# Performance work log

Hardware: AMD Instinct MI355X
Metric: run time of the kernel (lower is better)

The kernel has to match this reference:

```python
import jax, jax.numpy as jnp
import numpy as np

B, S, T = 32, 512, 512
SRC_SIZE, TGT_SIZE, OUT_SIZE, NUM_HEAD = 2048, 1024, 1024, 8
HEAD_DIM = OUT_SIZE // NUM_HEAD  # 128


def setup_inputs() -> dict:
    key = jax.random.key(0)
    ks = jax.random.split(key, 12)
    src = jax.random.normal(ks[0], (B, S, SRC_SIZE), dtype=jnp.float32)
    tgt = jax.random.normal(ks[1], (B, T, TGT_SIZE), dtype=jnp.float32)
    # binary float masks (1=valid, 0=pad); guarantee at least one valid src per row
    src_mask = (jax.random.uniform(ks[2], (B, S)) > 0.3).astype(jnp.float32)
    src_mask = src_mask.at[:, 0].set(1.0)
    tgt_mask = (jax.random.uniform(ks[3], (B, T)) > 0.3).astype(jnp.float32)
    tgt_mask = tgt_mask.at[:, 0].set(1.0)
    # FCNet in this repo is weight_norm(Linear) with no activation at drop=0 -> plain Linear
    def lin(k, out_f, in_f):
        return jax.random.normal(k, (out_f, in_f), dtype=jnp.float32) / np.sqrt(in_f)
    W_src = lin(ks[4], 2 * OUT_SIZE, SRC_SIZE)
    b_src = jnp.zeros((2 * OUT_SIZE,), jnp.float32)
    W_tgt = lin(ks[5], OUT_SIZE, TGT_SIZE)
    b_tgt = jnp.zeros((OUT_SIZE,), jnp.float32)
    W_out = lin(ks[6], OUT_SIZE, OUT_SIZE + TGT_SIZE)
    b_out = jnp.zeros((OUT_SIZE,), jnp.float32)
    return {"src": src, "tgt": tgt, "src_mask": src_mask, "tgt_mask": tgt_mask,
            "W_src": W_src, "b_src": b_src, "W_tgt": W_tgt, "b_tgt": b_tgt,
            "W_out": W_out, "b_out": b_out}


def reference(src, tgt, src_mask, tgt_mask, W_src, b_src, W_tgt, b_tgt, W_out, b_out):
    b, s, _ = src.shape
    t = tgt.shape[1]
    # projections (FCNet == Linear here)
    src_trans = jnp.einsum('bsf,of->bso', src, W_src) + b_src        # [B,S,2D]
    tgt_trans = jnp.einsum('btf,of->bto', tgt, W_tgt) + b_tgt        # [B,T,D]
    src_trans = src_trans * src_mask[:, :, None]
    tgt_trans = tgt_trans * tgt_mask[:, :, None]
    src_key, src_val = jnp.split(src_trans, 2, axis=2)               # each [B,S,D]
    # contiguous per-head chunks == reshape
    k = src_key.reshape(b, s, NUM_HEAD, HEAD_DIM)
    v = src_val.reshape(b, s, NUM_HEAD, HEAD_DIM)
    q = tgt_trans.reshape(b, t, NUM_HEAD, HEAD_DIM)
    scores = jnp.einsum('bthd,bshd->bhts', q, k) / np.sqrt(HEAD_DIM)  # [B,H,T,S]
    scores = jnp.where(src_mask[:, None, None, :] == 0, -jnp.inf, scores)
    attn = jax.nn.softmax(scores, axis=-1)
    tgt_update = jnp.einsum('bhts,bshd->bthd', attn, v).reshape(b, t, OUT_SIZE)
    cat_tgt = jnp.concatenate([tgt, tgt_update], axis=2)             # [B,T,TGT+D]
    return jnp.einsum('btf,of->bto', cat_tgt, W_out) + b_out         # [B,T,D]
```

## Files before the change

kernel.cpp:

```cpp
#include <hip/hip_runtime.h>

typedef __attribute__((ext_vector_type(4))) float f32x4;
typedef __attribute__((ext_vector_type(8))) short short8;
typedef unsigned short u16;

#define SB0() __builtin_amdgcn_sched_barrier(0)

__device__ __forceinline__ u16 f2bf(float f) {
  unsigned int u = __float_as_uint(f);
  return (u16)((u + 0x7fffu + ((u >> 16) & 1u)) >> 16);
}

__device__ __forceinline__ void gload16(const void* g, void* l) {
  __builtin_amdgcn_global_load_lds((const __attribute__((address_space(1))) void*)g,
                                   (__attribute__((address_space(3))) void*)l, 16, 0, 0);
}

__global__ void cvt_f32_bf16(const float* __restrict__ in, u16* __restrict__ out, int n4) {
  int i = blockIdx.x * blockDim.x + threadIdx.x;
  int stride = gridDim.x * blockDim.x;
  for (; i < n4; i += stride) {
    float4 v = ((const float4*)in)[i];
    ushort4 o;
    o.x = f2bf(v.x); o.y = f2bf(v.y); o.z = f2bf(v.z); o.w = f2bf(v.w);
    ((ushort4*)out)[i] = o;
  }
}

__global__ void cvt_tgt_strided(const float* __restrict__ in, u16* __restrict__ cat, int n4) {
  int i = blockIdx.x * blockDim.x + threadIdx.x;
  int stride = gridDim.x * blockDim.x;
  for (; i < n4; i += stride) {
    int e = i * 4;
    int row = e >> 10;
    int c = e & 1023;
    float4 v = ((const float4*)in)[i];
    ushort4 o;
    o.x = f2bf(v.x); o.y = f2bf(v.y); o.z = f2bf(v.z); o.w = f2bf(v.w);
    *(ushort4*)(cat + (size_t)row * 2048 + c) = o;
  }
}

template <bool MASK, bool OUTBF, bool VSPLIT>
__global__ __launch_bounds__(512) void gemm256(const u16* __restrict__ A, int lda,
                                               const u16* __restrict__ W,
                                               const float* __restrict__ bias,
                                               const float* __restrict__ rowmask,
                                               void* __restrict__ Cout, int ldc,
                                               int nbn, int K,
                                               u16* __restrict__ vTout) {
  __shared__ __align__(16) u16 lds[2 * 32768];
  const int tid = threadIdx.x;
  const int lane = tid & 63;
  const int wid = tid >> 6;
  const int lr = lane & 15, lh = lane >> 4;
  const int wm = wid >> 2;
  const int wn = wid & 3;

  const int nwg = gridDim.x;
  const int cpx = nwg >> 3;
  const int bid = (blockIdx.x & 7) * cpx + (blockIdx.x >> 3);
  const int bm = bid / nbn;
  const int bn = bid - bm * nbn;

  const int srow = tid >> 3;
  const int scol = ((tid & 7) ^ (srow & 7)) << 3;
  const u16* As0 = A + (size_t)(bm * 256 + srow) * lda + scol;
  const u16* Ws0 = W + (size_t)(bn * 256 + srow) * K + scol;

  auto stageA = [&](int h, int t, int buf) {
    char* d = (char*)lds + buf * 65536 + h * 16384 + tid * 16;
    const u16* s = As0 + (size_t)(h * 128) * lda + t * 64;
    gload16(s, d);
    gload16(s + (size_t)64 * lda, d + 8192);
  };
  auto stageB = [&](int h, int t, int buf) {
    char* d = (char*)lds + buf * 65536 + 32768 + h * 16384 + tid * 16;
    const u16* s = Ws0 + (size_t)(h * 128) * K + t * 64;
    gload16(s, d);
    gload16(s + (size_t)64 * K, d + 8192);
  };

  const int key = (lr & 7) << 4;
  const int sb0 = ((0 + lh) << 4) ^ key;
  const int sb1 = ((4 + lh) << 4) ^ key;
  const int arow = (wm * 64 + lr) * 128;
  const int brow = 32768 + (wn * 32 + lr) * 128;

  f32x4 acc[8][4];
#pragma unroll
  for (int m = 0; m < 8; ++m)
#pragma unroll
    for (int n = 0; n < 4; ++n) acc[m][n] = (f32x4){0.f, 0.f, 0.f, 0.f};

  const int NT = K >> 6;

  stageA(0, 0, 0); stageB(0, 0, 0); stageB(1, 0, 0); stageA(1, 0, 0);
  asm volatile("s_waitcnt vmcnt(0)" ::: "memory");
  __builtin_amdgcn_s_barrier();
  SB0();

  for (int t = 0; t < NT; ++t) {
    const int cur = t & 1, nxt = cur ^ 1;
    const char* Lb = (const char*)lds + cur * 65536;
    const bool pf = (t + 1 < NT);

    short8 a[4][2], a2[4][2], b0[2][2], b1[2][2];

#pragma unroll
    for (int m = 0; m < 4; ++m) {
      a[m][0] = *(const short8*)(Lb + arow + m * 2048 + sb0);
      a[m][1] = *(const short8*)(Lb + arow + m * 2048 + sb1);
    }
#pragma unroll
    for (int n = 0; n < 2; ++n) {
      b0[n][0] = *(const short8*)(Lb + brow + n * 2048 + sb0);
      b0[n][1] = *(const short8*)(Lb + brow + n * 2048 + sb1);
    }
    SB0();
    if (pf) { stageA(0, t + 1, nxt); stageB(0, t + 1, nxt);
              stageB(1, t + 1, nxt); stageA(1, t + 1, nxt); }
#pragma unroll
    for (int n = 0; n < 2; ++n) {
      b1[n][0] = *(const short8*)(Lb + brow + 16384 + n * 2048 + sb0);
      b1[n][1] = *(const short8*)(Lb + brow + 16384 + n * 2048 + sb1);
    }
    SB0();
    asm volatile("s_waitcnt lgkmcnt(4)" ::: "memory");
    SB0();
    __builtin_amdgcn_s_setprio(1);
#pragma unroll
    for (int m = 0; m < 4; ++m)
#pragma unroll
      for (int n = 0; n < 2; ++n) {
        acc[m][n] = __builtin_amdgcn_mfma_f32_16x16x32_bf16(a[m][0], b0[n][0], acc[m][n], 0, 0, 0);
        acc[m][n] = __builtin_amdgcn_mfma_f32_16x16x32_bf16(a[m][1], b0[n][1], acc[m][n], 0, 0, 0);
      }
    __builtin_amdgcn_s_setprio(0);
#pragma unroll
    for (int m = 0; m < 4; ++m) {
      a2[m][0] = *(const short8*)(Lb + 16384 + arow + m * 2048 + sb0);
      a2[m][1] = *(const short8*)(Lb + 16384 + arow + m * 2048 + sb1);
    }
    asm volatile("s_waitcnt lgkmcnt(8)" ::: "memory");
    SB0();
    __builtin_amdgcn_s_setprio(1);
#pragma unroll
    for (int m = 0; m < 4; ++m)
#pragma unroll
      for (int n = 0; n < 2; ++n) {
        acc[m][2 + n] = __builtin_amdgcn_mfma_f32_16x16x32_bf16(a[m][0], b1[n][0], acc[m][2 + n], 0, 0, 0);
        acc[m][2 + n] = __builtin_amdgcn_mfma_f32_16x16x32_bf16(a[m][1], b1[n][1], acc[m][2 + n], 0, 0, 0);
      }
    __builtin_amdgcn_s_setprio(0);
    asm volatile("s_waitcnt lgkmcnt(0)" ::: "memory");
    SB0();
    __builtin_amdgcn_s_setprio(1);
#pragma unroll
    for (int m = 0; m < 4; ++m)
#pragma unroll
      for (int n = 0; n < 2; ++n) {
        acc[4 + m][n] = __builtin_amdgcn_mfma_f32_16x16x32_bf16(a2[m][0], b0[n][0], acc[4 + m][n], 0, 0, 0);
        acc[4 + m][n] = __builtin_amdgcn_mfma_f32_16x16x32_bf16(a2[m][1], b0[n][1], acc[4 + m][n], 0, 0, 0);
      }
#pragma unroll
    for (int m = 0; m < 4; ++m)
#pragma unroll
      for (int n = 0; n < 2; ++n) {
        acc[4 + m][2 + n] = __builtin_amdgcn_mfma_f32_16x16x32_bf16(a2[m][0], b1[n][0], acc[4 + m][2 + n], 0, 0, 0);
        acc[4 + m][2 + n] = __builtin_amdgcn_mfma_f32_16x16x32_bf16(a2[m][1], b1[n][1], acc[4 + m][2 + n], 0, 0, 0);
      }
    __builtin_amdgcn_s_setprio(0);
    SB0();
    asm volatile("s_waitcnt vmcnt(0)" ::: "memory");
    __builtin_amdgcn_s_barrier();
    SB0();
  }

  const int r0 = bm * 256 + wm * 64 + lh * 4;
  const int c0 = bn * 256 + wn * 32 + lr;

  if constexpr (VSPLIT) {
    if (bn * 256 >= 1024) {
#pragma unroll
      for (int mi = 0; mi < 8; ++mi) {
        const int row_base = r0 + (mi >> 2) * 128 + (mi & 3) * 16;
        const int b = row_base >> 9;
        const int s = row_base & 511;
        float mk[4];
#pragma unroll
        for (int i = 0; i < 4; ++i) mk[i] = rowmask[row_base + i];
#pragma unroll
        for (int ni = 0; ni < 4; ++ni) {
          const int col = c0 + (ni >> 1) * 128 + (ni & 1) * 16;
          const float bv = bias[col];
          const int vcol = col - 1024;
          u16* vp = vTout + ((size_t)(b * 8 + (vcol >> 7)) * 128 + (vcol & 127)) * 512 + s;
          ushort4 o;
          o.x = f2bf((acc[mi][ni][0] + bv) * mk[0]);
          o.y = f2bf((acc[mi][ni][1] + bv) * mk[1]);
          o.z = f2bf((acc[mi][ni][2] + bv) * mk[2]);
          o.w = f2bf((acc[mi][ni][3] + bv) * mk[3]);
          *(ushort4*)vp = o;
        }
      }
      return;
    }
  }

#pragma unroll
  for (int mi = 0; mi < 8; ++mi) {
    const int row_base = r0 + (mi >> 2) * 128 + (mi & 3) * 16;
#pragma unroll
    for (int i = 0; i < 4; ++i) {
      const int row = row_base + i;
      float msk = 1.f;
      if constexpr (MASK) msk = rowmask[row];
#pragma unroll
      for (int ni = 0; ni < 4; ++ni) {
        const int col = c0 + (ni >> 1) * 128 + (ni & 1) * 16;
        float v = (acc[mi][ni][i] + bias[col]) * msk;
        if constexpr (OUTBF)
          ((u16*)Cout)[(size_t)row * ldc + col] = f2bf(v);
        else
          ((float*)Cout)[(size_t)row * ldc + col] = v;
      }
    }
  }
}

__global__ __launch_bounds__(256) void attn_fwd(const u16* __restrict__ q,
                                                const u16* __restrict__ kbuf,
                                                const u16* __restrict__ vT,
                                                const float* __restrict__ smask,
                                                u16* __restrict__ cat) {
  __shared__ __align__(16) u16 lds[20480];
  u16* Ks = lds;
  u16* Vt = lds + 8192;
  u16* Ps = lds + 16384;
  const int tid = threadIdx.x;
  const int lane = tid & 63;
  const int w = tid >> 6;
  const int lr = lane & 15, lh = lane >> 4;
  const int bh = blockIdx.x & 255;
  const int qb = blockIdx.x >> 8;
  const int b = bh >> 3;
  const int h = bh & 7;
  const int t0 = qb * 64 + w * 16;
  const float SCALE = 0.08838834764831845f;

  const u16* kbase = kbuf + (size_t)(b * 512) * 1024 + h * 128;
  const u16* vbase = vT + (size_t)bh * 128 * 512;

  short8 qf[4];
  {
    const u16* qp = q + (size_t)(b * 512 + t0 + lr) * 1024 + h * 128 + lh * 8;
#pragma unroll
    for (int kc = 0; kc < 4; ++kc) qf[kc] = *(const short8*)(qp + kc * 32);
  }

  f32x4 o[8];
#pragma unroll
  for (int dt = 0; dt < 8; ++dt) o[dt] = (f32x4){0.f, 0.f, 0.f, 0.f};
  float m_run[4], l_run[4];
#pragma unroll
  for (int i = 0; i < 4; ++i) { m_run[i] = -1e30f; l_run[i] = 0.f; }

  for (int s0 = 0; s0 < 512; s0 += 64) {
    __syncthreads();
#pragma unroll
    for (int it = 0; it < 4; ++it) {
      int idx = it * 256 + tid;
      int kr = idx >> 4, ks = idx & 15;
      gload16(kbase + (size_t)(s0 + kr) * 1024 + ((ks ^ (kr & 7)) * 8), (char*)Ks + idx * 16);
      int vr = idx >> 3, vs = idx & 7;
      gload16(vbase + (size_t)vr * 512 + s0 + ((vs ^ (vr & 7)) * 8), (char*)Vt + idx * 16);
    }
    asm volatile("s_waitcnt vmcnt(0)" ::: "memory");
    __syncthreads();

    f32x4 sc[4];
#pragma unroll
    for (int st = 0; st < 4; ++st) {
      f32x4 c = (f32x4){0.f, 0.f, 0.f, 0.f};
      const int row = st * 16 + lr;
#pragma unroll
      for (int kc = 0; kc < 4; ++kc) {
        short8 kb = *(const short8*)((const char*)Ks + row * 256 +
                                     ((kc * 64 + lh * 16) ^ ((row & 7) << 4)));
        c = __builtin_amdgcn_mfma_f32_16x16x32_bf16(qf[kc], kb, c, 0, 0, 0);
      }
      sc[st] = c;
    }

    float cm[4];
#pragma unroll
    for (int st = 0; st < 4; ++st) cm[st] = smask[b * 512 + s0 + st * 16 + lr];

    float pv[4][4], mx[4];
#pragma unroll
    for (int i = 0; i < 4; ++i) mx[i] = -1e30f;
#pragma unroll
    for (int st = 0; st < 4; ++st)
#pragma unroll
      for (int i = 0; i < 4; ++i) {
        float v = (cm[st] != 0.f) ? sc[st][i] * SCALE : -1e30f;
        pv[st][i] = v;
        mx[i] = fmaxf(mx[i], v);
      }
#pragma unroll
    for (int off = 1; off < 16; off <<= 1)
#pragma unroll
      for (int i = 0; i < 4; ++i) mx[i] = fmaxf(mx[i], __shfl_xor(mx[i], off));

    float m_new[4], scl[4], rs[4];
#pragma unroll
    for (int i = 0; i < 4; ++i) {
      m_new[i] = fmaxf(m_run[i], mx[i]);
      scl[i] = __expf(m_run[i] - m_new[i]);
      rs[i] = 0.f;
    }
#pragma unroll
    for (int st = 0; st < 4; ++st)
#pragma unroll
      for (int i = 0; i < 4; ++i) {
        float p = (cm[st] != 0.f) ? __expf(pv[st][i] - m_new[i]) : 0.f;
        pv[st][i] = p;
        rs[i] += p;
      }
#pragma unroll
    for (int off = 1; off < 16; off <<= 1)
#pragma unroll
      for (int i = 0; i < 4; ++i) rs[i] += __shfl_xor(rs[i], off);
#pragma unroll
    for (int i = 0; i < 4; ++i) {
      l_run[i] = l_run[i] * scl[i] + rs[i];
      m_run[i] = m_new[i];
    }
#pragma unroll
    for (int dt = 0; dt < 8; ++dt)
#pragma unroll
      for (int i = 0; i < 4; ++i) o[dt][i] *= scl[i];

#pragma unroll
    for (int st = 0; st < 4; ++st)
#pragma unroll
      for (int i = 0; i < 4; ++i) {
        const int prow = lh * 4 + i;
        Ps[w * 1024 + prow * 64 + (((st * 2 + (lr >> 3)) ^ (prow & 7)) * 8) + (lr & 7)] =
            f2bf(pv[st][i]);
      }

    short8 pa[2];
#pragma unroll
    for (int s2 = 0; s2 < 2; ++s2)
      pa[s2] = *(const short8*)(Ps + w * 1024 + lr * 64 + (((s2 * 4 + lh) ^ (lr & 7)) * 8));
#pragma unroll
    for (int dt = 0; dt < 8; ++dt) {
#pragma unroll
      for (int s2 = 0; s2 < 2; ++s2) {
        const int row = dt * 16 + lr;
        short8 vb = *(const short8*)((const char*)Vt + row * 128 +
                                     ((s2 * 64 + lh * 16) ^ ((row & 7) << 4)));
        o[dt] = __builtin_amdgcn_mfma_f32_16x16x32_bf16(pa[s2], vb, o[dt], 0, 0, 0);
      }
    }
  }

  float inv[4];
#pragma unroll
  for (int i = 0; i < 4; ++i) inv[i] = 1.f / l_run[i];
  u16* outp = cat + (size_t)(b * 512 + t0 + lh * 4) * 2048 + 1024 + h * 128 + lr;
#pragma unroll
  for (int dt = 0; dt < 8; ++dt)
#pragma unroll
    for (int i = 0; i < 4; ++i)
      outp[(size_t)i * 2048 + dt * 16] = f2bf(o[dt][i] * inv[i]);
}

extern "C" void kernel_launch(void* const* d_in, const int* in_sizes, int n_in,
                              void* d_out, int out_size, void* d_ws, size_t ws_size,
                              hipStream_t stream) {
  (void)in_sizes; (void)n_in; (void)out_size; (void)ws_size;
  const float* src      = (const float*)d_in[0];
  const float* tgt      = (const float*)d_in[1];
  const float* src_mask = (const float*)d_in[2];
  const float* tgt_mask = (const float*)d_in[3];
  const float* W_src    = (const float*)d_in[4];
  const float* b_src    = (const float*)d_in[5];
  const float* W_tgt    = (const float*)d_in[6];
  const float* b_tgt    = (const float*)d_in[7];
  const float* W_out    = (const float*)d_in[8];
  const float* b_out    = (const float*)d_in[9];

  char* ws = (char*)d_ws;
  u16* catb = (u16*)(ws);
  u16* kbuf = (u16*)(ws + 67108864);
  u16* vTb  = (u16*)(ws + 100663296);
  u16* qbuf = (u16*)(ws + 134217728);
  u16* wsrc = (u16*)(ws + 167772160);
  u16* wtgt = (u16*)(ws + 176160768);
  u16* wout = (u16*)(ws + 178257920);

  cvt_f32_bf16<<<2048, 256, 0, stream>>>(src, catb, 16384 * 2048 / 4);
  cvt_f32_bf16<<<1024, 256, 0, stream>>>(W_src, wsrc, 2048 * 2048 / 4);
  cvt_f32_bf16<<<256, 256, 0, stream>>>(W_tgt, wtgt, 1024 * 1024 / 4);
  cvt_f32_bf16<<<512, 256, 0, stream>>>(W_out, wout, 1024 * 2048 / 4);

  gemm256<true, true, true><<<512, 512, 0, stream>>>(catb, 2048, wsrc, b_src, src_mask,
                                                     kbuf, 1024, 8, 2048, vTb);

  cvt_tgt_strided<<<1024, 256, 0, stream>>>(tgt, catb, 16384 * 1024 / 4);

  gemm256<true, true, false><<<256, 512, 0, stream>>>(catb, 2048, wtgt, b_tgt, tgt_mask,
                                                      qbuf, 1024, 4, 1024, nullptr);

  attn_fwd<<<2048, 256, 0, stream>>>(qbuf, kbuf, vTb, src_mask, catb);

  gemm256<false, false, false><<<256, 512, 0, stream>>>(catb, 2048, wout, b_out, nullptr,
                                                        (float*)d_out, 1024, 4, 2048, nullptr);
}
```

Baseline: 384.2 us.

## Prefetch next-tile LDS fragments inside GEMM loop and enlarge attention blocks

The GEMM main loop is restructured so that the A and B0 register fragments for the next K tile are read from LDS during the current iteration, after an early barrier, instead of at the top of the next iteration. This is meant to hide LDS read latency behind the MFMAs. Separately, the attention kernel moves to 512-thread blocks covering 128 query rows, so each K/V tile staged in LDS is shared by twice as many queries and half as many blocks are launched. The attention change needs more LDS per block, which may lower occupancy, and the extra barrier placement in the GEMM adds synchronisation risk.

```diff
diff --git a/kernel.cpp b/kernel.cpp
--- a/kernel.cpp
+++ b/kernel.cpp
@@ -100,13 +100,9 @@
   __builtin_amdgcn_s_barrier();
   SB0();
 
-  for (int t = 0; t < NT; ++t) {
-    const int cur = t & 1, nxt = cur ^ 1;
-    const char* Lb = (const char*)lds + cur * 65536;
-    const bool pf = (t + 1 < NT);
-
-    short8 a[4][2], a2[4][2], b0[2][2], b1[2][2];
-
+  short8 a[4][2], a2[4][2], b0[2][2], b1[2][2];
+  {
+    const char* Lb = (const char*)lds;
 #pragma unroll
     for (int m = 0; m < 4; ++m) {
       a[m][0] = *(const short8*)(Lb + arow + m * 2048 + sb0);
@@ -118,8 +114,17 @@
       b0[n][1] = *(const short8*)(Lb + brow + n * 2048 + sb1);
     }
     SB0();
-    if (pf) { stageA(0, t + 1, nxt); stageB(0, t + 1, nxt);
+  }
+
+  for (int t = 0; t < NT; ++t) {
+    const int nxt = (t + 1) & 1;
+    const char* Lb = (const char*)lds + (t & 1) * 65536;
+    const char* Ln = (const char*)lds + nxt * 65536;
+    const bool ra = (t + 1 < NT);
+
+    if (ra) { stageA(0, t + 1, nxt); stageB(0, t + 1, nxt);
               stageB(1, t + 1, nxt); stageA(1, t + 1, nxt); }
+
 #pragma unroll
     for (int n = 0; n < 2; ++n) {
       b1[n][0] = *(const short8*)(Lb + brow + 16384 + n * 2048 + sb0);
@@ -137,11 +142,14 @@
         acc[m][n] = __builtin_amdgcn_mfma_f32_16x16x32_bf16(a[m][1], b0[n][1], acc[m][n], 0, 0, 0);
       }
     __builtin_amdgcn_s_setprio(0);
+    SB0();
+
 #pragma unroll
     for (int m = 0; m < 4; ++m) {
       a2[m][0] = *(const short8*)(Lb + 16384 + arow + m * 2048 + sb0);
       a2[m][1] = *(const short8*)(Lb + 16384 + arow + m * 2048 + sb1);
     }
+    SB0();
     asm volatile("s_waitcnt lgkmcnt(8)" ::: "memory");
     SB0();
     __builtin_amdgcn_s_setprio(1);
@@ -153,8 +161,24 @@
         acc[m][2 + n] = __builtin_amdgcn_mfma_f32_16x16x32_bf16(a[m][1], b1[n][1], acc[m][2 + n], 0, 0, 0);
       }
     __builtin_amdgcn_s_setprio(0);
-    asm volatile("s_waitcnt lgkmcnt(0)" ::: "memory");
-    SB0();
+    SB0();
+
+    if (ra) {
+      asm volatile("s_waitcnt vmcnt(0)" ::: "memory");
+      __builtin_amdgcn_s_barrier();
+      SB0();
+#pragma unroll
+      for (int m = 0; m < 4; ++m) {
+        a[m][0] = *(const short8*)(Ln + arow + m * 2048 + sb0);
+        a[m][1] = *(const short8*)(Ln + arow + m * 2048 + sb1);
+      }
+      SB0();
+      asm volatile("s_waitcnt lgkmcnt(8)" ::: "memory");
+      SB0();
+    } else {
+      asm volatile("s_waitcnt lgkmcnt(0)" ::: "memory");
+      SB0();
+    }
     __builtin_amdgcn_s_setprio(1);
 #pragma unroll
     for (int m = 0; m < 4; ++m)
@@ -163,6 +187,18 @@
         acc[4 + m][n] = __builtin_amdgcn_mfma_f32_16x16x32_bf16(a2[m][0], b0[n][0], acc[4 + m][n], 0, 0, 0);
         acc[4 + m][n] = __builtin_amdgcn_mfma_f32_16x16x32_bf16(a2[m][1], b0[n][1], acc[4 + m][n], 0, 0, 0);
       }
+    __builtin_amdgcn_s_setprio(0);
+    SB0();
+
+    if (ra) {
+#pragma unroll
+      for (int n = 0; n < 2; ++n) {
+        b0[n][0] = *(const short8*)(Ln + brow + n * 2048 + sb0);
+        b0[n][1] = *(const short8*)(Ln + brow + n * 2048 + sb1);
+      }
+      SB0();
+    }
+    __builtin_amdgcn_s_setprio(1);
 #pragma unroll
     for (int m = 0; m < 4; ++m)
 #pragma unroll
@@ -172,7 +208,6 @@
       }
     __builtin_amdgcn_s_setprio(0);
     SB0();
-    asm volatile("s_waitcnt vmcnt(0)" ::: "memory");
     __builtin_amdgcn_s_barrier();
     SB0();
   }
@@ -229,12 +264,12 @@
   }
 }
 
-__global__ __launch_bounds__(256) void attn_fwd(const u16* __restrict__ q,
+__global__ __launch_bounds__(512) void attn_fwd(const u16* __restrict__ q,
                                                 const u16* __restrict__ kbuf,
                                                 const u16* __restrict__ vT,
                                                 const float* __restrict__ smask,
                                                 u16* __restrict__ cat) {
-  __shared__ __align__(16) u16 lds[20480];
+  __shared__ __align__(16) u16 lds[24576];
   u16* Ks = lds;
   u16* Vt = lds + 8192;
   u16* Ps = lds + 16384;
@@ -246,7 +281,7 @@
   const int qb = blockIdx.x >> 8;
   const int b = bh >> 3;
   const int h = bh & 7;
-  const int t0 = qb * 64 + w * 16;
+  const int t0 = qb * 128 + w * 16;
   const float SCALE = 0.08838834764831845f;
 
   const u16* kbase = kbuf + (size_t)(b * 512) * 1024 + h * 128;
@@ -269,8 +304,8 @@
   for (int s0 = 0; s0 < 512; s0 += 64) {
     __syncthreads();
 #pragma unroll
-    for (int it = 0; it < 4; ++it) {
-      int idx = it * 256 + tid;
+    for (int it = 0; it < 2; ++it) {
+      int idx = it * 512 + tid;
       int kr = idx >> 4, ks = idx & 15;
       gload16(kbase + (size_t)(s0 + kr) * 1024 + ((ks ^ (kr & 7)) * 8), (char*)Ks + idx * 16);
       int vr = idx >> 3, vs = idx & 7;
@@ -415,7 +450,7 @@
   gemm256<true, true, false><<<256, 512, 0, stream>>>(catb, 2048, wtgt, b_tgt, tgt_mask,
                                                       qbuf, 1024, 4, 1024, nullptr);
 
-  attn_fwd<<<2048, 256, 0, stream>>>(qbuf, kbuf, vTb, src_mask, catb);
+  attn_fwd<<<1024, 512, 0, stream>>>(qbuf, kbuf, vTb, src_mask, catb);
 
   gemm256<false, false, false><<<256, 512, 0, stream>>>(catb, 2048, wout, b_out, nullptr,
                                                         (float*)d_out, 1024, 4, 2048, nullptr);
```

New measurement: 411.1 us. 1.07x slower.

## Pre-pack weights into MFMA fragment order and load B directly to registers

Applied to the files above, without the earlier changes.

Adds a pack_w kernel that converts the weight matrices to bf16 in the lane-ordered layout of the MFMA B operand. The GEMM then loads B fragments straight from global memory into registers, prefetched one step ahead, instead of staging them through LDS. This halves LDS use per block and removes the B LDS reads and writes. It also drops the XCD-aware block swizzle in favour of a simple bn/bm split. The risks are longer global-load latency on B, higher register pressure, and possibly worse L2 locality without the swizzle.

```diff
diff --git a/kernel.cpp b/kernel.cpp
--- a/kernel.cpp
+++ b/kernel.cpp
@@ -41,15 +41,34 @@
   }
 }
 
+__global__ void pack_w(const float* __restrict__ W, u16* __restrict__ Wp, int K, int total) {
+  int ci = blockIdx.x * 256 + threadIdx.x;
+  if (ci >= total) return;
+  int l = ci & 63;
+  int g = ci >> 6;
+  int K5 = K >> 5;
+  int np = g / K5;
+  int ksg = g - np * K5;
+  const float* s = W + (size_t)(np * 16 + (l & 15)) * K + ksg * 32 + (l >> 4) * 8;
+  float4 v0 = *(const float4*)s;
+  float4 v1 = *(const float4*)(s + 4);
+  u16* d = Wp + (size_t)ci * 8;
+  ushort4 o0, o1;
+  o0.x = f2bf(v0.x); o0.y = f2bf(v0.y); o0.z = f2bf(v0.z); o0.w = f2bf(v0.w);
+  o1.x = f2bf(v1.x); o1.y = f2bf(v1.y); o1.z = f2bf(v1.z); o1.w = f2bf(v1.w);
+  *(ushort4*)d = o0;
+  *(ushort4*)(d + 4) = o1;
+}
+
 template <bool MASK, bool OUTBF, bool VSPLIT>
 __global__ __launch_bounds__(512) void gemm256(const u16* __restrict__ A, int lda,
-                                               const u16* __restrict__ W,
+                                               const u16* __restrict__ Wp,
                                                const float* __restrict__ bias,
                                                const float* __restrict__ rowmask,
                                                void* __restrict__ Cout, int ldc,
-                                               int nbn, int K,
+                                               int nbnl, int K,
                                                u16* __restrict__ vTout) {
-  __shared__ __align__(16) u16 lds[2 * 32768];
+  __shared__ __align__(16) u16 lds[2 * 16384];
   const int tid = threadIdx.x;
   const int lane = tid & 63;
   const int wid = tid >> 6;
@@ -57,35 +76,34 @@
   const int wm = wid >> 2;
   const int wn = wid & 3;
 
-  const int nwg = gridDim.x;
-  const int cpx = nwg >> 3;
-  const int bid = (blockIdx.x & 7) * cpx + (blockIdx.x >> 3);
-  const int bm = bid / nbn;
-  const int bn = bid - bm * nbn;
+  const int bn = blockIdx.x & ((1 << nbnl) - 1);
+  const int bm = blockIdx.x >> nbnl;
 
   const int srow = tid >> 3;
   const int scol = ((tid & 7) ^ (srow & 7)) << 3;
   const u16* As0 = A + (size_t)(bm * 256 + srow) * lda + scol;
-  const u16* Ws0 = W + (size_t)(bn * 256 + srow) * K + scol;
-
-  auto stageA = [&](int h, int t, int buf) {
-    char* d = (char*)lds + buf * 65536 + h * 16384 + tid * 16;
-    const u16* s = As0 + (size_t)(h * 128) * lda + t * 64;
-    gload16(s, d);
-    gload16(s + (size_t)64 * lda, d + 8192);
+
+  auto stageA = [&](int t, int buf) {
+    char* d = (char*)lds + buf * 32768 + tid * 16;
+    const u16* s = As0 + t * 64;
+#pragma unroll
+    for (int i = 0; i < 4; ++i)
+      gload16(s + (size_t)(i * 64) * lda, d + i * 8192);
   };
-  auto stageB = [&](int h, int t, int buf) {
-    char* d = (char*)lds + buf * 65536 + 32768 + h * 16384 + tid * 16;
-    const u16* s = Ws0 + (size_t)(h * 128) * K + t * 64;
-    gload16(s, d);
-    gload16(s + (size_t)64 * K, d + 8192);
-  };
 
   const int key = (lr & 7) << 4;
-  const int sb0 = ((0 + lh) << 4) ^ key;
+  const int sb0 = (lh << 4) ^ key;
   const int sb1 = ((4 + lh) << 4) ^ key;
   const int arow = (wm * 64 + lr) * 128;
-  const int brow = 32768 + (wn * 32 + lr) * 128;
+
+  const int K5 = K >> 5;
+  const short8* Wp8 = (const short8*)Wp;
+  const short8* WB[2][2];
+#pragma unroll
+  for (int nh = 0; nh < 2; ++nh)
+#pragma unroll
+    for (int n = 0; n < 2; ++n)
+      WB[nh][n] = Wp8 + (size_t)(bn * 16 + nh * 8 + wn * 2 + n) * K5 * 64 + lane;
 
   f32x4 acc[8][4];
 #pragma unroll
@@ -95,55 +113,58 @@
 
   const int NT = K >> 6;
 
-  stageA(0, 0, 0); stageB(0, 0, 0); stageB(1, 0, 0); stageA(1, 0, 0);
+  short8 a[4][2], a2[4][2], b0[2][2], b1[2][2];
+
+  stageA(0, 0);
+  SB0();
+#pragma unroll
+  for (int n = 0; n < 2; ++n) {
+    b0[n][0] = WB[0][n][0];
+    b0[n][1] = WB[0][n][64];
+  }
+  SB0();
+#pragma unroll
+  for (int n = 0; n < 2; ++n) {
+    b1[n][0] = WB[1][n][0];
+    b1[n][1] = WB[1][n][64];
+  }
+  SB0();
   asm volatile("s_waitcnt vmcnt(0)" ::: "memory");
   __builtin_amdgcn_s_barrier();
   SB0();
 
   for (int t = 0; t < NT; ++t) {
-    const int cur = t & 1, nxt = cur ^ 1;
-    const char* Lb = (const char*)lds + cur * 65536;
+    const char* Lb = (const char*)lds + (t & 1) * 32768;
     const bool pf = (t + 1 < NT);
-
-    short8 a[4][2], a2[4][2], b0[2][2], b1[2][2];
 
 #pragma unroll
     for (int m = 0; m < 4; ++m) {
       a[m][0] = *(const short8*)(Lb + arow + m * 2048 + sb0);
       a[m][1] = *(const short8*)(Lb + arow + m * 2048 + sb1);
     }
-#pragma unroll
-    for (int n = 0; n < 2; ++n) {
-      b0[n][0] = *(const short8*)(Lb + brow + n * 2048 + sb0);
-      b0[n][1] = *(const short8*)(Lb + brow + n * 2048 + sb1);
-    }
-    SB0();
-    if (pf) { stageA(0, t + 1, nxt); stageB(0, t + 1, nxt);
-              stageB(1, t + 1, nxt); stageA(1, t + 1, nxt); }
-#pragma unroll
-    for (int n = 0; n < 2; ++n) {
-      b1[n][0] = *(const short8*)(Lb + brow + 16384 + n * 2048 + sb0);
-      b1[n][1] = *(const short8*)(Lb + brow + 16384 + n * 2048 + sb1);
-    }
-    SB0();
-    asm volatile("s_waitcnt lgkmcnt(4)" ::: "memory");
-    SB0();
-    __builtin_amdgcn_s_setprio(1);
-#pragma unroll
-    for (int m = 0; m < 4; ++m)
-#pragma unroll
-      for (int n = 0; n < 2; ++n) {
-        acc[m][n] = __builtin_amdgcn_mfma_f32_16x16x32_bf16(a[m][0], b0[n][0], acc[m][n], 0, 0, 0);
-        acc[m][n] = __builtin_amdgcn_mfma_f32_16x16x32_bf16(a[m][1], b0[n][1], acc[m][n], 0, 0, 0);
-      }
-    __builtin_amdgcn_s_setprio(0);
+    SB0();
 #pragma unroll
     for (int m = 0; m < 4; ++m) {
       a2[m][0] = *(const short8*)(Lb + 16384 + arow + m * 2048 + sb0);
       a2[m][1] = *(const short8*)(Lb + 16384 + arow + m * 2048 + sb1);
     }
+    SB0();
+    if (pf) stageA(t + 1, (t + 1) & 1);
+    SB0();
+
     asm volatile("s_waitcnt lgkmcnt(8)" ::: "memory");
     SB0();
+    __builtin_amdgcn_s_setprio(1);
+#pragma unroll
+    for (int m = 0; m < 4; ++m)
+#pragma unroll
+      for (int n = 0; n < 2; ++n) {
+        acc[m][n] = __builtin_amdgcn_mfma_f32_16x16x32_bf16(a[m][0], b0[n][0], acc[m][n], 0, 0, 0);
+        acc[m][n] = __builtin_amdgcn_mfma_f32_16x16x32_bf16(a[m][1], b0[n][1], acc[m][n], 0, 0, 0);
+      }
+    __builtin_amdgcn_s_setprio(0);
+    SB0();
+
     __builtin_amdgcn_s_setprio(1);
 #pragma unroll
     for (int m = 0; m < 4; ++m)
@@ -153,6 +174,8 @@
         acc[m][2 + n] = __builtin_amdgcn_mfma_f32_16x16x32_bf16(a[m][1], b1[n][1], acc[m][2 + n], 0, 0, 0);
       }
     __builtin_amdgcn_s_setprio(0);
+    SB0();
+
     asm volatile("s_waitcnt lgkmcnt(0)" ::: "memory");
     SB0();
     __builtin_amdgcn_s_setprio(1);
@@ -163,6 +186,20 @@
         acc[4 + m][n] = __builtin_amdgcn_mfma_f32_16x16x32_bf16(a2[m][0], b0[n][0], acc[4 + m][n], 0, 0, 0);
         acc[4 + m][n] = __builtin_amdgcn_mfma_f32_16x16x32_bf16(a2[m][1], b0[n][1], acc[4 + m][n], 0, 0, 0);
       }
+    __builtin_amdgcn_s_setprio(0);
+    SB0();
+
+    if (pf) {
+      const int o = (2 * (t + 1)) * 64;
+#pragma unroll
+      for (int n = 0; n < 2; ++n) {
+        b0[n][0] = WB[0][n][o];
+        b0[n][1] = WB[0][n][o + 64];
+      }
+      SB0();
+    }
+
+    __builtin_amdgcn_s_setprio(1);
 #pragma unroll
     for (int m = 0; m < 4; ++m)
 #pragma unroll
@@ -172,6 +209,17 @@
       }
     __builtin_amdgcn_s_setprio(0);
     SB0();
+
+    if (pf) {
+      const int o = (2 * (t + 1)) * 64;
+#pragma unroll
+      for (int n = 0; n < 2; ++n) {
+        b1[n][0] = WB[1][n][o];
+        b1[n][1] = WB[1][n][o + 64];
+      }
+      SB0();
+    }
+
     asm volatile("s_waitcnt vmcnt(0)" ::: "memory");
     __builtin_amdgcn_s_barrier();
     SB0();
@@ -403,20 +451,20 @@
   u16* wout = (u16*)(ws + 178257920);
 
   cvt_f32_bf16<<<2048, 256, 0, stream>>>(src, catb, 16384 * 2048 / 4);
-  cvt_f32_bf16<<<1024, 256, 0, stream>>>(W_src, wsrc, 2048 * 2048 / 4);
-  cvt_f32_bf16<<<256, 256, 0, stream>>>(W_tgt, wtgt, 1024 * 1024 / 4);
-  cvt_f32_bf16<<<512, 256, 0, stream>>>(W_out, wout, 1024 * 2048 / 4);
+  pack_w<<<2048, 256, 0, stream>>>(W_src, wsrc, 2048, 2048 * 2048 / 8);
+  pack_w<<<512, 256, 0, stream>>>(W_tgt, wtgt, 1024, 1024 * 1024 / 8);
+  pack_w<<<1024, 256, 0, stream>>>(W_out, wout, 2048, 1024 * 2048 / 8);
 
   gemm256<true, true, true><<<512, 512, 0, stream>>>(catb, 2048, wsrc, b_src, src_mask,
-                                                     kbuf, 1024, 8, 2048, vTb);
+                                                     kbuf, 1024, 3, 2048, vTb);
 
   cvt_tgt_strided<<<1024, 256, 0, stream>>>(tgt, catb, 16384 * 1024 / 4);
 
   gemm256<true, true, false><<<256, 512, 0, stream>>>(catb, 2048, wtgt, b_tgt, tgt_mask,
-                                                      qbuf, 1024, 4, 1024, nullptr);
+                                                      qbuf, 1024, 2, 1024, nullptr);
 
   attn_fwd<<<2048, 256, 0, stream>>>(qbuf, kbuf, vTb, src_mask, catb);
 
   gemm256<false, false, false><<<256, 512, 0, stream>>>(catb, 2048, wout, b_out, nullptr,
-                                                        (float*)d_out, 1024, 4, 2048, nullptr);
-}
+                                                        (float*)d_out, 1024, 2, 2048, nullptr);
+}
```

Result: slower. 410.9 us, median of 2 (+7.0%).
